# Performance work log

Measured on AMD Instinct MI355X. Metric: run time of the kernel, lower is better.

Reference implementation:

```python
import jax, jax.numpy as jnp
import numpy as np

TAU = 20.0   # membrane time constant (init default)
TH = 1.0     # spike threshold (init default)
K = 10.0     # surrogate sigmoid slope (hard-coded in forward)
EPS = 1e-6


def setup_inputs() -> dict:
    key = jax.random.key(0)
    I = jax.random.normal(key, (4096, 4096), dtype=jnp.float32)  # [B, L]
    return {"I": I}


def reference(I):
    B, L = I.shape

    def step(v, I_t):
        # Euler: dv = -v/tau + I ; v <- v + dv
        v = v - v / TAU + I_t
        s_soft = jax.nn.sigmoid(K * (v - TH))
        s_hard = (v >= TH).astype(I.dtype)
        # straight-through: value = s_hard, gradient flows through s_soft
        s = jax.lax.stop_gradient(s_hard - s_soft) + s_soft
        # reset: v <- v * (1 - stopgrad(s)); stopgrad(s) has value s_hard
        v = v * (1.0 - s_hard)
        return v, (s, s_hard)

    v0 = jnp.zeros((B,), dtype=I.dtype)
    _, (spikes_t, hard_t) = jax.lax.scan(step, v0, I.T)  # xs: [L, B]
    spikes = spikes_t.T       # [B, L]
    hard_spikes = hard_t.T    # [B, L]

    # hard latency: index of first hard spike, else L
    fired = hard_spikes > 0.5
    has = jnp.any(fired, axis=1)
    idx = jnp.argmax(fired, axis=1)
    hard_latency = jnp.where(has, idx, L).astype(jnp.int32)  # [B]

    # soft latency: spike-weighted mean time
    time = jnp.arange(L, dtype=spikes.dtype)
    w = spikes / (spikes.sum(axis=1, keepdims=True) + EPS)
    soft_latency = (w * time).sum(axis=1)  # [B]

    return spikes, hard_latency, soft_latency
```

## Files before the change

### kernel.cpp

```cpp
#include <hip/hip_runtime.h>

#define B_DIM 4096
#define L_DIM 4096
#define SEGLEN 256
#define NSEG (L_DIM / SEGLEN)
#define WARM 512
#define CHUNK 64
#define CF4 (CHUNK / 4)
#define LSTRIDE 68

__global__ __launch_bounds__(256) void init_kernel(float* wsf, int* wsi) {
    int i = blockIdx.x * 256 + threadIdx.x;
    if (i < 2 * B_DIM) wsf[i] = 0.f;
    if (i < B_DIM) wsi[i] = L_DIM;
}

#define LIF_CORE(IIN)                         \
    float q0 = u * cdiv;                      \
    float rr = fmaf(-20.0f, q0, u);           \
    float q  = fmaf(rr, cdiv, q0);            \
    float a  = u - q;                         \
    float b  = a + (IIN);                     \
    u = sp ? (IIN) : b;                       \
    sp = (u >= 1.0f);

#define WARM_STEP(IIN) { LIF_CORE(IIN) }

#define FULL_STEP(IIN, SOUT)                  \
    {                                         \
        LIF_CORE(IIN)                         \
        float sf = sp ? 1.0f : 0.0f;          \
        cnt += sf;                            \
        seen = fmaxf(seen, sf);               \
        accS += cnt;                          \
        accF += seen;                         \
        (SOUT) = sf;                          \
    }

__global__ __launch_bounds__(128, 1) void lif_kernel(const float* __restrict__ I,
                                                     float* __restrict__ out,
                                                     float* __restrict__ Cacc,
                                                     float* __restrict__ tsAcc,
                                                     int* __restrict__ firstAcc) {
    __shared__ __align__(16) float lds[2][64 * LSTRIDE];
    const int wid = threadIdx.x >> 6;
    const int lane = threadIdx.x & 63;
    const int seg = blockIdx.x >> 6;
    const int rowBase = (blockIdx.x & 63) * 64;
    const int t0 = seg * SEGLEN;
    const int start = (t0 > WARM) ? (t0 - WARM) : 0;
    const int nwarmCh = (t0 - start) / CHUNK;
    const int nch = nwarmCh + SEGLEN / CHUNK;

    if (wid == 1) {
        const int srow = lane >> 4, scol = lane & 15;
        const float* gb = I + (size_t)rowBase * L_DIM + start + scol * 4;
        float* ob = out + (size_t)rowBase * L_DIM + t0 + scol * 4;
        {
            float* dst = &lds[0][0];
#pragma unroll
            for (int p = 0; p < 16; ++p) {
                const int r = 4 * p + srow;
                float4 v = *(const float4*)(gb + (size_t)r * L_DIM);
                *(float4*)&dst[r * LSTRIDE + scol * 4] = v;
            }
        }
        __syncthreads();
        for (int c = 0; c < nch; ++c) {
            const int cp = c - 1;
            if (cp >= nwarmCh) {
                float* sb = &lds[cp & 1][0];
                float4 S[16];
#pragma unroll
                for (int p = 0; p < 16; ++p) {
                    const int r = 4 * p + srow;
                    S[p] = *(const float4*)&sb[r * LSTRIDE + scol * 4];
                }
                float* og = ob + (size_t)(cp - nwarmCh) * CHUNK;
#pragma unroll
                for (int p = 0; p < 16; ++p) {
                    const int r = 4 * p + srow;
                    *(float4*)(og + (size_t)r * L_DIM) = S[p];
                }
            }
            if (c + 1 < nch) {
                const float* g = gb + (c + 1) * CHUNK;
                float* dst = &lds[(c + 1) & 1][0];
#pragma unroll
                for (int p = 0; p < 16; ++p) {
                    const int r = 4 * p + srow;
                    float4 v = *(const float4*)(g + (size_t)r * L_DIM);
                    *(float4*)&dst[r * LSTRIDE + scol * 4] = v;
                }
            }
            __syncthreads();
        }
        {
            const int cp = nch - 1;
            float* sb = &lds[cp & 1][0];
            float* og = ob + (size_t)(cp - nwarmCh) * CHUNK;
#pragma unroll
            for (int p = 0; p < 16; ++p) {
                const int r = 4 * p + srow;
                float4 v = *(const float4*)&sb[r * LSTRIDE + scol * 4];
                *(float4*)(og + (size_t)r * L_DIM) = v;
            }
        }
    } else {
        const int row = rowBase + lane;
        float u = 0.f, cnt = 0.f, seen = 0.f, accS = 0.f, accF = 0.f;
        bool sp = false;
        const float cdiv = 0.05f;

        __syncthreads();
        for (int c = 0; c < nch; ++c) {
            float* buf = &lds[c & 1][lane * LSTRIDE];
            float4 R[CF4];
#pragma unroll
            for (int j = 0; j < CF4; ++j) R[j] = *(const float4*)(buf + 4 * j);

            if (c < nwarmCh) {
#pragma unroll
                for (int j = 0; j < CF4; ++j) {
                    float4 iv = R[j];
                    WARM_STEP(iv.x) WARM_STEP(iv.y) WARM_STEP(iv.z) WARM_STEP(iv.w)
                }
            } else {
#pragma unroll
                for (int j = 0; j < CF4; ++j) {
                    float4 iv = R[j];
                    float4 sv;
                    FULL_STEP(iv.x, sv.x) FULL_STEP(iv.y, sv.y)
                    FULL_STEP(iv.z, sv.z) FULL_STEP(iv.w, sv.w)
                    *(float4*)(buf + 4 * j) = sv;
                }
            }
            __syncthreads();
        }

        if (cnt > 0.f) {
            const int firstLocal = (int)((float)SEGLEN - accF);
            atomicMin(&firstAcc[row], t0 + firstLocal);
        }
        atomicAdd(&Cacc[row], cnt);
        atomicAdd(&tsAcc[row], fmaf((float)(t0 + SEGLEN), cnt, -accS));
    }
}

__global__ __launch_bounds__(256) void fin_kernel(const float* __restrict__ Cacc,
                                                  const float* __restrict__ tsAcc,
                                                  const int* __restrict__ firstAcc,
                                                  float* __restrict__ out) {
    int r = blockIdx.x * 256 + threadIdx.x;
    if (r < B_DIM) {
        out[(size_t)B_DIM * L_DIM + r] = (float)firstAcc[r];
        out[(size_t)B_DIM * L_DIM + B_DIM + r] = tsAcc[r] / (Cacc[r] + 1e-6f);
    }
}

extern "C" void kernel_launch(void* const* d_in, const int* in_sizes, int n_in,
                              void* d_out, int out_size, void* d_ws, size_t ws_size,
                              hipStream_t stream) {
    const float* I = (const float*)d_in[0];
    float* out = (float*)d_out;
    float* wsf = (float*)d_ws;
    int* wsi = (int*)((float*)d_ws + 2 * B_DIM);
    (void)in_sizes; (void)n_in; (void)out_size; (void)ws_size;

    init_kernel<<<(2 * B_DIM + 255) / 256, 256, 0, stream>>>(wsf, wsi);
    lif_kernel<<<NSEG * 64, 128, 0, stream>>>(I, out, wsf, wsf + B_DIM, wsi);
    fin_kernel<<<(B_DIM + 255) / 256, 256, 0, stream>>>(wsf, wsf + B_DIM, wsi, out);
}
```

Baseline: 129.9 us.

## Prefetch input chunks two ahead in registers and use LDS-only barriers

The copy wave now issues global loads for chunk c+2 into a register double-buffer before doing the LDS-to-global store of the previous chunk and the LDS write of the next one. This keeps more global loads in flight and overlaps them with the stores. Block barriers are replaced by an lgkmcnt-only wait plus s_barrier, so outstanding vector-memory loads no longer drain at each sync. The cost is doubled register usage for the staging buffers, and the code relies on an even chunk count for the unrolled two-phase loop.

```diff
diff --git a/kernel.cpp b/kernel.cpp
--- a/kernel.cpp
+++ b/kernel.cpp
@@ -37,6 +37,11 @@
         (SOUT) = sf;                          \
     }
 
+#define BARRIER_SYNC()                                      \
+    asm volatile("s_waitcnt lgkmcnt(0)" ::: "memory");      \
+    __builtin_amdgcn_s_barrier();                           \
+    __builtin_amdgcn_sched_barrier(0);
+
 __global__ __launch_bounds__(128, 1) void lif_kernel(const float* __restrict__ I,
                                                      float* __restrict__ out,
                                                      float* __restrict__ Cacc,
@@ -56,48 +61,69 @@
         const int srow = lane >> 4, scol = lane & 15;
         const float* gb = I + (size_t)rowBase * L_DIM + start + scol * 4;
         float* ob = out + (size_t)rowBase * L_DIM + t0 + scol * 4;
+        float4 Ga[16], Gb[16];
+
+#pragma unroll
+        for (int p = 0; p < 16; ++p)
+            Ga[p] = *(const float4*)(gb + (size_t)(4 * p + srow) * L_DIM);
+        if (1 < nch) {
+            const float* g = gb + CHUNK;
+#pragma unroll
+            for (int p = 0; p < 16; ++p)
+                Gb[p] = *(const float4*)(g + (size_t)(4 * p + srow) * L_DIM);
+        }
         {
             float* dst = &lds[0][0];
 #pragma unroll
-            for (int p = 0; p < 16; ++p) {
-                const int r = 4 * p + srow;
-                float4 v = *(const float4*)(gb + (size_t)r * L_DIM);
-                *(float4*)&dst[r * LSTRIDE + scol * 4] = v;
+            for (int p = 0; p < 16; ++p)
+                *(float4*)&dst[(4 * p + srow) * LSTRIDE + scol * 4] = Ga[p];
+        }
+        BARRIER_SYNC();
+
+        auto phase = [&](const int c, float4 (&Gld)[16], float4 (&Gwr)[16]) {
+            if (c + 2 < nch) {
+                const float* g = gb + (c + 2) * CHUNK;
+#pragma unroll
+                for (int p = 0; p < 16; ++p)
+                    Gld[p] = *(const float4*)(g + (size_t)(4 * p + srow) * L_DIM);
             }
-        }
-        __syncthreads();
-        for (int c = 0; c < nch; ++c) {
+            __builtin_amdgcn_sched_barrier(0);
             const int cp = c - 1;
             if (cp >= nwarmCh) {
-                float* sb = &lds[cp & 1][0];
-                float4 S[16];
-#pragma unroll
-                for (int p = 0; p < 16; ++p) {
-                    const int r = 4 * p + srow;
-                    S[p] = *(const float4*)&sb[r * LSTRIDE + scol * 4];
-                }
+                const float* sb = &lds[cp & 1][0];
                 float* og = ob + (size_t)(cp - nwarmCh) * CHUNK;
 #pragma unroll
-                for (int p = 0; p < 16; ++p) {
-                    const int r = 4 * p + srow;
-                    *(float4*)(og + (size_t)r * L_DIM) = S[p];
+                for (int g4 = 0; g4 < 4; ++g4) {
+                    float4 S[4];
+#pragma unroll
+                    for (int q = 0; q < 4; ++q) {
+                        const int r = 4 * (4 * g4 + q) + srow;
+                        S[q] = *(const float4*)&sb[r * LSTRIDE + scol * 4];
+                    }
+#pragma unroll
+                    for (int q = 0; q < 4; ++q) {
+                        const int r = 4 * (4 * g4 + q) + srow;
+                        *(float4*)(og + (size_t)r * L_DIM) = S[q];
+                    }
                 }
             }
             if (c + 1 < nch) {
-                const float* g = gb + (c + 1) * CHUNK;
                 float* dst = &lds[(c + 1) & 1][0];
 #pragma unroll
-                for (int p = 0; p < 16; ++p) {
-                    const int r = 4 * p + srow;
-                    float4 v = *(const float4*)(g + (size_t)r * L_DIM);
-                    *(float4*)&dst[r * LSTRIDE + scol * 4] = v;
-                }
+                for (int p = 0; p < 16; ++p)
+                    *(float4*)&dst[(4 * p + srow) * LSTRIDE + scol * 4] = Gwr[p];
             }
-            __syncthreads();
+            BARRIER_SYNC();
+        };
+
+        for (int c = 0; c < nch; c += 2) {
+            phase(c, Ga, Gb);
+            phase(c + 1, Gb, Ga);
         }
+
         {
             const int cp = nch - 1;
-            float* sb = &lds[cp & 1][0];
+            const float* sb = &lds[cp & 1][0];
             float* og = ob + (size_t)(cp - nwarmCh) * CHUNK;
 #pragma unroll
             for (int p = 0; p < 16; ++p) {
@@ -112,7 +138,7 @@
         bool sp = false;
         const float cdiv = 0.05f;
 
-        __syncthreads();
+        BARRIER_SYNC();
         for (int c = 0; c < nch; ++c) {
             float* buf = &lds[c & 1][lane * LSTRIDE];
             float4 R[CF4];
@@ -135,7 +161,7 @@
                     *(float4*)(buf + 4 * j) = sv;
                 }
             }
-            __syncthreads();
+            BARRIER_SYNC();
         }
 
         if (cnt > 0.f) {
```

Measured after the change: 193.8 us. 1.49x slower.
